# Kernel optimization log

Measured on AMD Instinct MI355X. Metric: run time of the kernel, lower is better.

## Reference

```python
import jax, jax.numpy as jnp
import numpy as np

D_MODEL = 1024
N_OCTAVES = 3


def _index_maps(d_model: int, n_octaves: int):
    """Static octave index maps, matching HarmonicMixing._build_index_maps."""
    maps = []
    for octave in range(1, n_octaves + 1):
        stride = 2 ** octave
        up_src = np.arange(d_model // stride)
        up_tgt = up_src * stride                      # i -> i*stride
        down_src = np.arange(stride, d_model)
        down_tgt = down_src // stride                 # i -> i // stride (many-to-one)
        maps.append((up_src, up_tgt, down_src, down_tgt))
    return maps


def setup_inputs() -> dict:
    key = jax.random.key(0)
    k1, k2, k3 = jax.random.split(key, 3)
    x = jax.random.normal(k1, (8, 4096, D_MODEL), dtype=jnp.float32)
    up_weights = jax.random.uniform(k2, (N_OCTAVES,), dtype=jnp.float32)
    down_weights = jax.random.uniform(k3, (N_OCTAVES,), dtype=jnp.float32)
    return {"x": x, "up_weights": up_weights, "down_weights": down_weights}


def reference(x, up_weights, down_weights):
    d_model = x.shape[-1]
    maps = _index_maps(d_model, N_OCTAVES)
    out = x
    for o, (up_src, up_tgt, down_src, down_tgt) in enumerate(maps):
        up_w = jax.nn.sigmoid(up_weights[o])
        down_w = jax.nn.sigmoid(down_weights[o])
        # gather -> scale -> scatter-add (duplicate targets accumulate)
        out = out.at[..., up_tgt].add(up_w * x[..., up_src])
        out = out.at[..., down_tgt].add(down_w * x[..., down_src])
    return out
```

## Files before the change

kernel.cpp:

```cpp
#include <hip/hip_runtime.h>


constexpr int D = 1024;

__global__ __launch_bounds__(256) void harmonic_kernel(
    const float* __restrict__ x,
    const float* __restrict__ uwp,
    const float* __restrict__ dwp,
    float* __restrict__ out)
{
    __shared__ float row[D];
    const int t = threadIdx.x;
    const long long base = (long long)blockIdx.x * D;

    const float uw0 = 1.f / (1.f + __expf(-uwp[0]));
    const float uw1 = 1.f / (1.f + __expf(-uwp[1]));
    const float uw2 = 1.f / (1.f + __expf(-uwp[2]));
    const float dw0 = 1.f / (1.f + __expf(-dwp[0]));
    const float dw1 = 1.f / (1.f + __expf(-dwp[1]));
    const float dw2 = 1.f / (1.f + __expf(-dwp[2]));

    const int j0 = t * 4;
    const float4 v = *reinterpret_cast<const float4*>(x + base + j0);
    *reinterpret_cast<float4*>(&row[j0]) = v;
    __syncthreads();

    float4 r = v;

    r.x += uw0 * row[j0 >> 1];
    r.z += uw0 * row[(j0 >> 1) + 1];
    r.x += uw1 * row[j0 >> 2];
    if ((j0 & 7) == 0) r.x += uw2 * row[j0 >> 3];

    if (j0 < 512) {
        const float4 a = *reinterpret_cast<const float4*>(&row[2 * j0]);
        const float4 b = *reinterpret_cast<const float4*>(&row[2 * j0 + 4]);
        if (j0 > 0) r.x += dw0 * (a.x + a.y);
        r.y += dw0 * (a.z + a.w);
        r.z += dw0 * (b.x + b.y);
        r.w += dw0 * (b.z + b.w);
    }
    if (j0 < 256) {
        const float4 a = *reinterpret_cast<const float4*>(&row[4 * j0]);
        const float4 b = *reinterpret_cast<const float4*>(&row[4 * j0 + 4]);
        const float4 c = *reinterpret_cast<const float4*>(&row[4 * j0 + 8]);
        const float4 d = *reinterpret_cast<const float4*>(&row[4 * j0 + 12]);
        if (j0 > 0) r.x += dw1 * (a.x + a.y + a.z + a.w);
        r.y += dw1 * (b.x + b.y + b.z + b.w);
        r.z += dw1 * (c.x + c.y + c.z + c.w);
        r.w += dw1 * (d.x + d.y + d.z + d.w);
    }
    if (j0 < 128) {
        const float* p = &row[8 * j0];
        float s[4];
        #pragma unroll
        for (int k = 0; k < 4; ++k) {
            const float4 a = *reinterpret_cast<const float4*>(p + 8 * k);
            const float4 b = *reinterpret_cast<const float4*>(p + 8 * k + 4);
            s[k] = (a.x + a.y + a.z + a.w) + (b.x + b.y + b.z + b.w);
        }
        if (j0 > 0) r.x += dw2 * s[0];
        r.y += dw2 * s[1];
        r.z += dw2 * s[2];
        r.w += dw2 * s[3];
    }

    *reinterpret_cast<float4*>(out + base + j0) = r;
}

extern "C" void kernel_launch(void* const* d_in, const int* in_sizes, int n_in,
                              void* d_out, int out_size, void* d_ws, size_t ws_size,
                              hipStream_t stream) {
    const float* x   = (const float*)d_in[0];
    const float* uwp = (const float*)d_in[1];
    const float* dwp = (const float*)d_in[2];
    float* out = (float*)d_out;
    const int n_rows = in_sizes[0] / D;
    harmonic_kernel<<<n_rows, 256, 0, stream>>>(x, uwp, dwp, out);
}
```

Measured before the change: 223.7 us.

## Precompute pairwise partial sums in registers and share via LDS

Each thread computes the 2-, 4- and 8-element partial sums of its float4 in registers, using a lane shuffle for the 8-sum. These sums go into small shared arrays, so the down-mixing terms become single float4 LDS reads instead of many row reads and adds. Only the lower half of the row is staged for the up-mixing gathers. This cuts LDS traffic and ALU work, but the kernel is likely bound by HBM bandwidth, so the gain may be small.

```diff
diff --git a/kernel.cpp b/kernel.cpp
--- a/kernel.cpp
+++ b/kernel.cpp
@@ -9,7 +9,11 @@
     const float* __restrict__ dwp,
     float* __restrict__ out)
 {
-    __shared__ float row[D];
+    __shared__ float rowlo[512];
+    __shared__ float S1[512];
+    __shared__ float S2[256];
+    __shared__ float S3[128];
+
     const int t = threadIdx.x;
     const long long base = (long long)blockIdx.x * D;
 
@@ -22,47 +26,46 @@
 
     const int j0 = t * 4;
     const float4 v = *reinterpret_cast<const float4*>(x + base + j0);
-    *reinterpret_cast<float4*>(&row[j0]) = v;
+
+    const float s1a = v.x + v.y;
+    const float s1b = v.z + v.w;
+    const float s2  = s1a + s1b;
+    const float s3  = s2 + __shfl_xor(s2, 1);
+
+    if (t < 128) *reinterpret_cast<float4*>(&rowlo[j0]) = v;
+    *reinterpret_cast<float2*>(&S1[2 * t]) = make_float2(s1a, s1b);
+    S2[t] = s2;
+    if ((t & 1) == 0) S3[t >> 1] = s3;
     __syncthreads();
 
     float4 r = v;
 
-    r.x += uw0 * row[j0 >> 1];
-    r.z += uw0 * row[(j0 >> 1) + 1];
-    r.x += uw1 * row[j0 >> 2];
-    if ((j0 & 7) == 0) r.x += uw2 * row[j0 >> 3];
+    const float2 u01 = *reinterpret_cast<const float2*>(&rowlo[2 * t]);
+    r.x += uw0 * u01.x;
+    r.z += uw0 * u01.y;
+    r.x += uw1 * rowlo[t];
+    if ((t & 1) == 0) r.x += uw2 * rowlo[t >> 1];
 
-    if (j0 < 512) {
-        const float4 a = *reinterpret_cast<const float4*>(&row[2 * j0]);
-        const float4 b = *reinterpret_cast<const float4*>(&row[2 * j0 + 4]);
-        if (j0 > 0) r.x += dw0 * (a.x + a.y);
-        r.y += dw0 * (a.z + a.w);
-        r.z += dw0 * (b.x + b.y);
-        r.w += dw0 * (b.z + b.w);
-    }
-    if (j0 < 256) {
-        const float4 a = *reinterpret_cast<const float4*>(&row[4 * j0]);
-        const float4 b = *reinterpret_cast<const float4*>(&row[4 * j0 + 4]);
-        const float4 c = *reinterpret_cast<const float4*>(&row[4 * j0 + 8]);
-        const float4 d = *reinterpret_cast<const float4*>(&row[4 * j0 + 12]);
-        if (j0 > 0) r.x += dw1 * (a.x + a.y + a.z + a.w);
-        r.y += dw1 * (b.x + b.y + b.z + b.w);
-        r.z += dw1 * (c.x + c.y + c.z + c.w);
-        r.w += dw1 * (d.x + d.y + d.z + d.w);
-    }
-    if (j0 < 128) {
-        const float* p = &row[8 * j0];
-        float s[4];
-        #pragma unroll
-        for (int k = 0; k < 4; ++k) {
-            const float4 a = *reinterpret_cast<const float4*>(p + 8 * k);
-            const float4 b = *reinterpret_cast<const float4*>(p + 8 * k + 4);
-            s[k] = (a.x + a.y + a.z + a.w) + (b.x + b.y + b.z + b.w);
+    if (t < 128) {
+        const float4 a = *reinterpret_cast<const float4*>(&S1[j0]);
+        if (t > 0) r.x += dw0 * a.x;
+        r.y += dw0 * a.y;
+        r.z += dw0 * a.z;
+        r.w += dw0 * a.w;
+        if (t < 64) {
+            const float4 b = *reinterpret_cast<const float4*>(&S2[j0]);
+            if (t > 0) r.x += dw1 * b.x;
+            r.y += dw1 * b.y;
+            r.z += dw1 * b.z;
+            r.w += dw1 * b.w;
+            if (t < 32) {
+                const float4 c = *reinterpret_cast<const float4*>(&S3[j0]);
+                if (t > 0) r.x += dw2 * c.x;
+                r.y += dw2 * c.y;
+                r.z += dw2 * c.z;
+                r.w += dw2 * c.w;
+            }
         }
-        if (j0 > 0) r.x += dw2 * s[0];
-        r.y += dw2 * s[1];
-        r.z += dw2 * s[2];
-        r.w += dw2 * s[3];
     }
 
     *reinterpret_cast<float4*>(out + base + j0) = r;
```

New measurement: 220.5 us. About the same (-1.4%).
